# Kernel optimization log

Measured on AMD Instinct MI355X. Metric: run time of the kernel, lower is better.

Reference implementation:

```python
import jax, jax.numpy as jnp
import numpy as np


def setup_inputs() -> dict:
    key = jax.random.key(0)
    D, B, F_in, H = 8, 256, 64, 128  # depth, n_trees, n_node_features, n_hidden
    S = 2 ** D - 1                    # nodes per complete binary tree = 255
    N = B * S                         # 65280 total nodes
    # Tree structure (heap layout, root = local node 0; children of i are 2i+1, 2i+2)
    idx = np.arange(S)
    level = np.floor(np.log2(idx + 1)).astype(np.int64)      # 0 at root .. D-1 at leaves
    node_order_single = (D - 1) - level                       # leaves evaluated first (order 0)
    child_local = np.arange(1, S)
    parent_local = (child_local - 1) // 2
    offs = (np.arange(B) * S)[:, None]
    parent_g = (parent_local[None, :] + offs).reshape(-1)
    child_g = (child_local[None, :] + offs).reshape(-1)
    ks = jax.random.split(key, 8)

    def w(k, shp, fan_in):
        return (jax.random.normal(k, shp, jnp.float32) / np.sqrt(np.float32(fan_in)))

    return {
        "features": jax.random.normal(ks[0], (N, F_in), jnp.float32),
        "W_iou": w(ks[1], (F_in, 3 * H), F_in),
        "b_iou": jnp.zeros((3 * H,), jnp.float32),
        "U_iou": w(ks[2], (H, 3 * H), H),
        "W_f": w(ks[3], (F_in, H), F_in),
        "b_f": jnp.zeros((H,), jnp.float32),
        "U_f": w(ks[4], (H, H), H),
        "lin1_w": w(ks[5], (H, H), H),
        "lin1_b": jnp.zeros((H,), jnp.float32),
        "lin2_w": w(ks[6], (H, H), H),
        "lin2_b": jnp.zeros((H,), jnp.float32),
        "lin_w": w(ks[7], (H, 1), H),
        "lin_b": jnp.zeros((1,), jnp.float32),
        "node_order": jnp.asarray(np.tile(node_order_single, B), jnp.int32),
        "adjacency_list": jnp.asarray(np.stack([parent_g, child_g], axis=1), jnp.int32),
        "edge_order": jnp.asarray(np.tile(node_order_single[parent_local], B), jnp.int32),
        "n_levels": int(D),
        "n_trees": int(B),
    }


def reference(features, W_iou, b_iou, U_iou, W_f, b_f, U_f,
              lin1_w, lin1_b, lin2_w, lin2_b, lin_w, lin_b,
              node_order, adjacency_list, edge_order, n_levels, n_trees):
    N = features.shape[0]
    H = U_f.shape[0]
    parent = adjacency_list[:, 0]
    child = adjacency_list[:, 1]
    # input-to-gate projections are level-independent; compute once
    Wx_iou = features @ W_iou + b_iou   # [N, 3H]
    Wx_f = features @ W_f + b_f         # [N, H]
    h = jnp.zeros((N, H), features.dtype)
    c = jnp.zeros((N, H), features.dtype)
    for lvl in range(n_levels):  # n_levels is a static Python int
        nmask = (node_order == lvl)[:, None]
        if lvl == 0:
            iou = Wx_iou
            c_sum = jnp.zeros((N, H), features.dtype)
        else:
            emask = (edge_order == lvl)[:, None]
            child_h = jnp.where(emask, h[child], 0.0)
            h_sum = jax.ops.segment_sum(child_h, parent, num_segments=N)  # sum child h per parent
            iou = Wx_iou + h_sum @ U_iou
            f = jax.nn.sigmoid(Wx_f[parent] + h[child] @ U_f)             # per-edge forget gate
            fc = jnp.where(emask, f * c[child], 0.0)
            c_sum = jax.ops.segment_sum(fc, parent, num_segments=N)
        i, o, u = jnp.split(iou, 3, axis=1)
        c_new = jax.nn.sigmoid(i) * jnp.tanh(u) + c_sum
        h_new = jax.nn.sigmoid(o) * jnp.tanh(c_new)
        h = jnp.where(nmask, h_new, h)
        c = jnp.where(nmask, c_new, c)
    # unbatch by (equal) tree sizes and mean-pool per tree (use_root=False)
    S = N // n_trees
    x = h.reshape(n_trees, S, H).mean(axis=1)
    x = jax.nn.relu(x)                                   # dropout: identity in eval
    x = jax.nn.relu(x @ lin1_w + lin1_b)
    x = jax.nn.relu(x @ lin2_w + lin2_b)
    out = (x @ lin_w + lin_b).reshape(-1)                # torch.flatten(x)
    return out
```

## Files before the change

### kernel.cpp

```cpp
#include <hip/hip_runtime.h>
#include <hip/hip_bf16.h>
#include <math.h>

#define S_NODES 255
#define B_TREES 256
#define F_IN 64
#define H_DIM 128

typedef __attribute__((ext_vector_type(8))) short short8;
typedef __attribute__((ext_vector_type(4))) float f32x4;

__device__ __forceinline__ float fsig(float x) {
    float e = __expf(-x);
    return __builtin_amdgcn_rcpf(1.0f + e);
}
__device__ __forceinline__ float ftanh_(float x) {
    x = fminf(fmaxf(x, -15.0f), 15.0f);
    float e = __expf(2.0f * x);
    return (e - 1.0f) * __builtin_amdgcn_rcpf(e + 1.0f);
}
__device__ __forceinline__ unsigned short f2bf(float x) {
    union { __hip_bfloat16 b; unsigned short u; } v; v.b = __float2bfloat16(x); return v.u;
}
__device__ __forceinline__ float bf2f(unsigned short u) {
    union { unsigned int w; float f; } v; v.w = ((unsigned int)u) << 16; return v.f;
}
__device__ __forceinline__ unsigned int packsplit(float x) {
    unsigned short hi = f2bf(x);
    unsigned short lo = f2bf(x - bf2f(hi));
    return (unsigned)hi | ((unsigned)lo << 16);
}
__device__ __forceinline__ float unpacksplit(unsigned int u) {
    return bf2f((unsigned short)(u & 0xffffu)) + bf2f((unsigned short)(u >> 16));
}

__global__ __launch_bounds__(256) void prep_bt(
    const float* __restrict__ U_iou, const float* __restrict__ U_f,
    const float* __restrict__ W_iou, const float* __restrict__ W_f,
    unsigned short* __restrict__ Btu, unsigned short* __restrict__ Btl)
{
    int t = blockIdx.x * 256 + threadIdx.x;
    if (t < 512 * 192) {
        int k = t >> 9, n = t & 511;
        float v;
        if (k < 128) v = (n < 384) ? U_iou[k * 384 + n] : U_f[k * 128 + (n - 384)];
        else {
            int kf = k - 128;
            v = (n < 384) ? 0.5f * W_iou[kf * 384 + n] : W_f[kf * 128 + (n - 384)];
        }
        unsigned short hi = f2bf(v);
        Btu[n * 384 + k] = hi;
        Btu[n * 384 + 192 + k] = f2bf(v - bf2f(hi));
    } else {
        int t2 = t - 512 * 192;
        int k = t2 & 63, n = t2 >> 6;
        float v = W_iou[k * 384 + n];
        unsigned short hi = f2bf(v);
        Btl[n * 128 + k] = hi;
        Btl[n * 128 + 64 + k] = f2bf(v - bf2f(hi));
    }
}

__global__ __launch_bounds__(256) void pack_weights(
    const float* __restrict__ W_iou, const float* __restrict__ W_f,
    const float* __restrict__ U_iou, const float* __restrict__ U_f,
    float4* __restrict__ Wp, float4* __restrict__ Up)
{
    int t = blockIdx.x * 256 + threadIdx.x;
    if (t < F_IN * H_DIM) {
        int k = t >> 7, j = t & 127;
        Wp[t] = make_float4(W_iou[k * 384 + j], W_iou[k * 384 + 128 + j],
                            W_iou[k * 384 + 256 + j], W_f[k * H_DIM + j]);
    } else {
        int t2 = t - F_IN * H_DIM;
        int k = t2 >> 7, j = t2 & 127;
        Up[t2] = make_float4(U_iou[k * 384 + j], U_iou[k * 384 + 128 + j],
                             U_iou[k * 384 + 256 + j], U_f[k * H_DIM + j]);
    }
}

#define MFMA(a, b, c) __builtin_amdgcn_mfma_f32_16x16x32_bf16(a, b, c, 0, 0, 0)

__global__ __launch_bounds__(512, 2) void leafgemm(
    const float* __restrict__ feat, const unsigned short* __restrict__ Btl,
    const float* __restrict__ b_iou,
    float* __restrict__ c_out, unsigned int* __restrict__ h2out)
{
    __shared__ __align__(16) char Alb[64 * 272];
    const int tid = threadIdx.x;
    const int w = tid >> 6, l = tid & 63;
    const int l15 = l & 15, l4 = l >> 4;
    const int NB = blockIdx.x << 6;

    int nct[3];
    #pragma unroll
    for (int ct = 0; ct < 3; ++ct) nct[ct] = (ct << 7) + (w << 4) + l15;

    short8 Bh[2][3], Bl[2][3];
    #define LLOADB(buf, ss) { int chb = ((ss) << 2) + l4;                         \
        _Pragma("unroll") for (int ct = 0; ct < 3; ++ct) {                        \
            const char* bp = (const char*)Btl + (size_t)nct[ct] * 256 + (chb << 4); \
            Bh[buf][ct] = *(const short8*)(bp);                                   \
            Bl[buf][ct] = *(const short8*)(bp + 128); } }

    LLOADB(0, 0)

    {
        int row = tid >> 3, o = tid & 7;
        int leafidx = NB + row;
        int tree = leafidx >> 7;
        size_t grow = (size_t)(tree * S_NODES + 127 + (leafidx & 127));
        const float* fp = feat + grow * F_IN + (o << 3);
        float4 va = *(const float4*)(fp);
        float4 vb = *(const float4*)(fp + 4);
        float vv[8] = {va.x, va.y, va.z, va.w, vb.x, vb.y, vb.z, vb.w};
        unsigned int qh[4], ql[4];
        #pragma unroll
        for (int e = 0; e < 4; ++e) {
            unsigned short h0 = f2bf(vv[2*e]), h1 = f2bf(vv[2*e+1]);
            unsigned short s0 = f2bf(vv[2*e] - bf2f(h0));
            unsigned short s1 = f2bf(vv[2*e+1] - bf2f(h1));
            qh[e] = (unsigned)h0 | ((unsigned)h1 << 16);
            ql[e] = (unsigned)s0 | ((unsigned)s1 << 16);
        }
        char* arow = Alb + row * 272;
        *(uint4*)(arow + (o << 4)) = make_uint4(qh[0], qh[1], qh[2], qh[3]);
        *(uint4*)(arow + ((8 + o) << 4)) = make_uint4(ql[0], ql[1], ql[2], ql[3]);
    }
    __syncthreads();

    f32x4 acc[4][3];
    #pragma unroll
    for (int rt = 0; rt < 4; ++rt)
        #pragma unroll
        for (int ct = 0; ct < 3; ++ct) acc[rt][ct] = (f32x4){0,0,0,0};

    #pragma unroll
    for (int s = 0; s < 2; ++s) {
        const int cur = s & 1;
        if (s < 1) LLOADB(1, 1)
        int ch = (s << 2) + l4;
        short8 ah[4], al[4];
        #pragma unroll
        for (int rt = 0; rt < 4; ++rt) {
            const char* ap = Alb + (rt * 16 + l15) * 272;
            ah[rt] = *(const short8*)(ap + (ch << 4));
            al[rt] = *(const short8*)(ap + ((8 + ch) << 4));
        }
        #pragma unroll
        for (int ct = 0; ct < 3; ++ct)
            #pragma unroll
            for (int rt = 0; rt < 4; ++rt) {
                acc[rt][ct] = MFMA(ah[rt], Bh[cur][ct], acc[rt][ct]);
                acc[rt][ct] = MFMA(al[rt], Bh[cur][ct], acc[rt][ct]);
                acc[rt][ct] = MFMA(ah[rt], Bl[cur][ct], acc[rt][ct]);
            }
    }

    const int j = (w << 4) + l15;
    float bi = b_iou[j], bo = b_iou[128 + j], bu = b_iou[256 + j];
    #pragma unroll
    for (int rt = 0; rt < 4; ++rt)
        #pragma unroll
        for (int rr = 0; rr < 4; ++rr) {
            int leafrow = rt * 16 + (l4 << 2) + rr;
            int leafidx = NB + leafrow;
            int tree = leafidx >> 7;
            size_t grow = (size_t)(tree * S_NODES + 127 + (leafidx & 127));
            float iv = acc[rt][0][rr] + bi;
            float ov = acc[rt][1][rr] + bo;
            float uv = acc[rt][2][rr] + bu;
            float cn = fsig(iv) * ftanh_(uv);
            float hn = fsig(ov) * ftanh_(cn);
            c_out[grow * 128 + j] = cn;
            h2out[grow * 128 + j] = packsplit(hn);
        }
    #undef LLOADB
}

__global__ __launch_bounds__(512, 2) void ugemm(
    const float* __restrict__ feat, const unsigned int* __restrict__ h2,
    const unsigned short* __restrict__ Btu,
    const float* __restrict__ b_iou, const float* __restrict__ b_f,
    float* __restrict__ c_io, unsigned int* __restrict__ h2out,
    int Lstart, int Lbits)
{
    __shared__ __align__(16) char Alb[64 * 784];
    const int tid = threadIdx.x;
    const int w = tid >> 6, l = tid & 63;
    const int l15 = l & 15, l4 = l >> 4;
    const int NB = blockIdx.x << 5;
    const int mask = (1 << Lbits) - 1;

    int nct[4];
    #pragma unroll
    for (int ct = 0; ct < 4; ++ct)
        nct[ct] = ((ct < 3) ? (ct << 7) : 384) + (w << 4) + l15;

    short8 Bh[2][4], Bl[2][4];
    #define ULOADB(buf, ss) { int chb = ((ss) << 2) + l4;                         \
        _Pragma("unroll") for (int ct = 0; ct < 4; ++ct) {                        \
            const char* bp = (const char*)Btu + (size_t)nct[ct] * 768 + (chb << 4); \
            Bh[buf][ct] = *(const short8*)(bp);                                   \
            Bl[buf][ct] = *(const short8*)(bp + 384); } }

    ULOADB(0, 0)

    #pragma unroll
    for (int i = 0; i < 2; ++i) {
        int tsk = tid + (i << 9);
        int row = tsk >> 4, o = tsk & 15;
        int node = NB + (row >> 1);
        int tree = node >> Lbits;
        int local = Lstart + (node & mask);
        size_t growc = (size_t)(tree * S_NODES + 2 * local + 1 + (row & 1));
        const unsigned int* hp = h2 + growc * 128 + (o << 3);
        uint4 a = *(const uint4*)(hp);
        uint4 b = *(const uint4*)(hp + 4);
        uint4 vh, vl;
        vh.x = (a.x & 0xffffu) | (a.y << 16);
        vh.y = (a.z & 0xffffu) | (a.w << 16);
        vh.z = (b.x & 0xffffu) | (b.y << 16);
        vh.w = (b.z & 0xffffu) | (b.w << 16);
        vl.x = (a.x >> 16) | (a.y & 0xffff0000u);
        vl.y = (a.z >> 16) | (a.w & 0xffff0000u);
        vl.z = (b.x >> 16) | (b.y & 0xffff0000u);
        vl.w = (b.z >> 16) | (b.w & 0xffff0000u);
        char* arow = Alb + row * 784;
        *(uint4*)(arow + (o << 4)) = vh;
        *(uint4*)(arow + ((24 + o) << 4)) = vl;
    }
    {
        int t2 = tid;
        int row = t2 >> 3, o = t2 & 7;
        int node = NB + (row >> 1);
        int tree = node >> Lbits;
        int local = Lstart + (node & mask);
        size_t growp = (size_t)(tree * S_NODES + local);
        const float* fp = feat + growp * F_IN + (o << 3);
        float4 va = *(const float4*)(fp);
        float4 vb = *(const float4*)(fp + 4);
        float vv[8] = {va.x, va.y, va.z, va.w, vb.x, vb.y, vb.z, vb.w};
        unsigned int qh[4], ql[4];
        #pragma unroll
        for (int e = 0; e < 4; ++e) {
            unsigned short h0 = f2bf(vv[2*e]), h1 = f2bf(vv[2*e+1]);
            unsigned short s0 = f2bf(vv[2*e] - bf2f(h0));
            unsigned short s1 = f2bf(vv[2*e+1] - bf2f(h1));
            qh[e] = (unsigned)h0 | ((unsigned)h1 << 16);
            ql[e] = (unsigned)s0 | ((unsigned)s1 << 16);
        }
        char* arow = Alb + row * 784;
        *(uint4*)(arow + ((16 + o) << 4)) = make_uint4(qh[0], qh[1], qh[2], qh[3]);
        *(uint4*)(arow + ((40 + o) << 4)) = make_uint4(ql[0], ql[1], ql[2], ql[3]);
    }
    __syncthreads();

    f32x4 acc[4][4];
    #pragma unroll
    for (int rt = 0; rt < 4; ++rt)
        #pragma unroll
        for (int ct = 0; ct < 4; ++ct) acc[rt][ct] = (f32x4){0,0,0,0};

    #pragma unroll
    for (int s = 0; s < 6; ++s) {
        const int cur = s & 1;
        if (s < 5) ULOADB(cur ^ 1, s + 1)
        int ch = (s << 2) + l4;
        short8 ah[4], al[4];
        #pragma unroll
        for (int rt = 0; rt < 4; ++rt) {
            const char* ap = Alb + (rt * 16 + l15) * 784;
            ah[rt] = *(const short8*)(ap + (ch << 4));
            al[rt] = *(const short8*)(ap + ((24 + ch) << 4));
        }
        #pragma unroll
        for (int ct = 0; ct < 4; ++ct)
            #pragma unroll
            for (int rt = 0; rt < 4; ++rt) {
                acc[rt][ct] = MFMA(ah[rt], Bh[cur][ct], acc[rt][ct]);
                acc[rt][ct] = MFMA(al[rt], Bh[cur][ct], acc[rt][ct]);
                acc[rt][ct] = MFMA(ah[rt], Bl[cur][ct], acc[rt][ct]);
            }
    }

    const int j = (w << 4) + l15;
    float bi = b_iou[j], bo = b_iou[128 + j], bu = b_iou[256 + j], bfv = b_f[j];
    #pragma unroll
    for (int rt = 0; rt < 4; ++rt)
        #pragma unroll
        for (int p = 0; p < 2; ++p) {
            int m = rt * 8 + (l4 << 1) + p;
            int node = NB + m;
            int tree = node >> Lbits;
            int local = Lstart + (node & mask);
            size_t gp = (size_t)(tree * S_NODES + local);
            size_t gl = (size_t)(tree * S_NODES + 2 * local + 1);
            float iv = acc[rt][0][2*p] + acc[rt][0][2*p+1] + bi;
            float ov = acc[rt][1][2*p] + acc[rt][1][2*p+1] + bo;
            float uv = acc[rt][2][2*p] + acc[rt][2][2*p+1] + bu;
            float fl = fsig(acc[rt][3][2*p] + bfv);
            float fr = fsig(acc[rt][3][2*p+1] + bfv);
            float cl = c_io[gl * 128 + j];
            float cr = c_io[(gl + 1) * 128 + j];
            float cn = fsig(iv) * ftanh_(uv) + fl * cl + fr * cr;
            float hn = fsig(ov) * ftanh_(cn);
            c_io[gp * 128 + j] = cn;
            h2out[gp * 128 + j] = packsplit(hn);
        }
    #undef ULOADB
}

#define ULOOP(KB, KE, HLROW, HRROW)                                             \
    _Pragma("unroll 2")                                                         \
    for (int k4 = (KB); k4 < (KE); k4 += 4) {                                   \
        float4 u0 = Up[(k4 + 0) * H_DIM + j];                                   \
        float4 u1 = Up[(k4 + 1) * H_DIM + j];                                   \
        float4 u2 = Up[(k4 + 2) * H_DIM + j];                                   \
        float4 u3 = Up[(k4 + 3) * H_DIM + j];                                   \
        _Pragma("unroll")                                                       \
        for (int g = 0; g < G; ++g) {                                           \
            float4 hl4 = *reinterpret_cast<const float4*>((HLROW) + k4);        \
            float4 hr4 = *reinterpret_cast<const float4*>((HRROW) + k4);        \
            float hs_;                                                          \
            hs_ = hl4.x + hr4.x;                                                \
            acc_i[g] = fmaf(hs_, u0.x, acc_i[g]);                               \
            acc_o[g] = fmaf(hs_, u0.y, acc_o[g]);                               \
            acc_u[g] = fmaf(hs_, u0.z, acc_u[g]);                               \
            acc_fl[g] = fmaf(hl4.x, u0.w, acc_fl[g]);                           \
            acc_fr[g] = fmaf(hr4.x, u0.w, acc_fr[g]);                           \
            hs_ = hl4.y + hr4.y;                                                \
            acc_i[g] = fmaf(hs_, u1.x, acc_i[g]);                               \
            acc_o[g] = fmaf(hs_, u1.y, acc_o[g]);                               \
            acc_u[g] = fmaf(hs_, u1.z, acc_u[g]);                               \
            acc_fl[g] = fmaf(hl4.y, u1.w, acc_fl[g]);                           \
            acc_fr[g] = fmaf(hr4.y, u1.w, acc_fr[g]);                           \
            hs_ = hl4.z + hr4.z;                                                \
            acc_i[g] = fmaf(hs_, u2.x, acc_i[g]);                               \
            acc_o[g] = fmaf(hs_, u2.y, acc_o[g]);                               \
            acc_u[g] = fmaf(hs_, u2.z, acc_u[g]);                               \
            acc_fl[g] = fmaf(hl4.z, u2.w, acc_fl[g]);                           \
            acc_fr[g] = fmaf(hr4.z, u2.w, acc_fr[g]);                           \
            hs_ = hl4.w + hr4.w;                                                \
            acc_i[g] = fmaf(hs_, u3.x, acc_i[g]);                               \
            acc_o[g] = fmaf(hs_, u3.y, acc_o[g]);                               \
            acc_u[g] = fmaf(hs_, u3.z, acc_u[g]);                               \
            acc_fl[g] = fmaf(hl4.w, u3.w, acc_fl[g]);                           \
            acc_fr[g] = fmaf(hr4.w, u3.w, acc_fr[g]);                           \
        }                                                                       \
    }

#define WLOOP(FS, WITH_F)                                                       \
    _Pragma("unroll 2")                                                         \
    for (int k4 = 0; k4 < F_IN; k4 += 4) {                                      \
        float4 w0 = Wp[(k4 + 0) * H_DIM + j];                                   \
        float4 w1 = Wp[(k4 + 1) * H_DIM + j];                                   \
        float4 w2 = Wp[(k4 + 2) * H_DIM + j];                                   \
        float4 w3 = Wp[(k4 + 3) * H_DIM + j];                                   \
        _Pragma("unroll")                                                       \
        for (int g = 0; g < G; ++g) {                                           \
            float4 f4 = *reinterpret_cast<const float4*>((FS) + g * F_IN + k4); \
            acc_i[g] = fmaf(f4.x, w0.x, acc_i[g]);                              \
            acc_o[g] = fmaf(f4.x, w0.y, acc_o[g]);                              \
            acc_u[g] = fmaf(f4.x, w0.z, acc_u[g]);                              \
            if (WITH_F) acc_f[g] = fmaf(f4.x, w0.w, acc_f[g]);                  \
            acc_i[g] = fmaf(f4.y, w1.x, acc_i[g]);                              \
            acc_o[g] = fmaf(f4.y, w1.y, acc_o[g]);                              \
            acc_u[g] = fmaf(f4.y, w1.z, acc_u[g]);                              \
            if (WITH_F) acc_f[g] = fmaf(f4.y, w1.w, acc_f[g]);                  \
            acc_i[g] = fmaf(f4.z, w2.x, acc_i[g]);                              \
            acc_o[g] = fmaf(f4.z, w2.y, acc_o[g]);                              \
            acc_u[g] = fmaf(f4.z, w2.z, acc_u[g]);                              \
            if (WITH_F) acc_f[g] = fmaf(f4.z, w2.w, acc_f[g]);                  \
            acc_i[g] = fmaf(f4.w, w3.x, acc_i[g]);                              \
            acc_o[g] = fmaf(f4.w, w3.y, acc_o[g]);                              \
            acc_u[g] = fmaf(f4.w, w3.z, acc_u[g]);                              \
            if (WITH_F) acc_f[g] = fmaf(f4.w, w3.w, acc_f[g]);                  \
        }                                                                       \
    }

__global__ __launch_bounds__(256) void tree_top_kernel(
    const float* __restrict__ feat, const float4* __restrict__ Wp,
    const float* __restrict__ b_iou, const float4* __restrict__ Up,
    const float* __restrict__ b_f,
    unsigned int* __restrict__ h2g, float* __restrict__ c)
{
    const int tree = blockIdx.x;
    const int tid = threadIdx.x;
    const int j = tid & 127;
    const int grp = tid >> 7;

    __shared__ float h_s[31][H_DIM];
    __shared__ float c_s[31][H_DIM];
    __shared__ float feat_s[2 * 4 * F_IN];
    __shared__ float red5[5][H_DIM];

    for (int idx = tid; idx < 16 * H_DIM; idx += 256) {
        int loc = 15 + (idx >> 7);
        int col = idx & 127;
        size_t n = (size_t)(tree * S_NODES + loc);
        h_s[loc][col] = unpacksplit(h2g[n * H_DIM + col]);
        c_s[loc][col] = c[n * H_DIM + col];
    }
    __syncthreads();

    float bi = b_iou[j], bo = b_iou[128 + j], bu = b_iou[256 + j], bf = b_f[j];

    #define TOP_SLOT(G_, BASE_)                                                      \
    {                                                                                \
        constexpr int G = G_;                                                        \
        const int base = BASE_;                                                      \
        for (int idx = tid; idx < 2 * G * F_IN; idx += 256) {                        \
            int gg = idx >> 6, kk = idx & 63;                                        \
            int local = base + gg;                                                   \
            feat_s[idx] = feat[(size_t)(tree * S_NODES + local) * F_IN + kk];        \
        }                                                                            \
        __syncthreads();                                                             \
        float acc_i[G], acc_o[G], acc_u[G], acc_f[G], acc_fl[G], acc_fr[G];          \
        _Pragma("unroll")                                                            \
        for (int g = 0; g < G; ++g) {                                                \
            acc_i[g] = bi; acc_o[g] = bo; acc_u[g] = bu;                             \
            acc_f[g] = bf; acc_fl[g] = 0.f; acc_fr[g] = 0.f;                         \
        }                                                                            \
        const float* fs = feat_s + grp * G * F_IN;                                   \
        WLOOP(fs, true)                                                              \
        ULOOP(0, H_DIM, &h_s[2 * (base + grp * G + g) + 1][0],                       \
                         &h_s[2 * (base + grp * G + g) + 2][0])                      \
        _Pragma("unroll")                                                            \
        for (int g = 0; g < G; ++g) {                                                \
            int p = base + grp * G + g;                                              \
            float cl = c_s[2 * p + 1][j];                                            \
            float cr = c_s[2 * p + 2][j];                                            \
            float cn = fsig(acc_i[g]) * ftanh_(acc_u[g]);                            \
            float fl = fsig(acc_f[g] + acc_fl[g]);                                   \
            float fr = fsig(acc_f[g] + acc_fr[g]);                                   \
            cn = fmaf(fl, cl, fmaf(fr, cr, cn));                                     \
            float hn = fsig(acc_o[g]) * ftanh_(cn);                                  \
            h_s[p][j] = hn;                                                          \
            c_s[p][j] = cn;                                                          \
            h2g[(size_t)(tree * S_NODES + p) * H_DIM + j] = packsplit(hn);           \
        }                                                                            \
        __syncthreads();                                                             \
    }

    TOP_SLOT(4, 7)
    TOP_SLOT(2, 3)
    TOP_SLOT(1, 1)
    #undef TOP_SLOT

    {
        constexpr int G = 1;
        constexpr int KS = 44;
        if (tid < F_IN) feat_s[tid] = feat[(size_t)(tree * S_NODES) * F_IN + tid];
        __syncthreads();
        float acc_i[1], acc_o[1], acc_u[1], acc_f[1], acc_fl[1], acc_fr[1];
        if (grp == 0) {
            acc_i[0] = bi; acc_o[0] = bo; acc_u[0] = bu;
            acc_f[0] = bf; acc_fl[0] = 0.f; acc_fr[0] = 0.f;
            WLOOP(feat_s, true)
            ULOOP(0, KS, &h_s[1][0], &h_s[2][0])
        } else {
            acc_i[0] = 0.f; acc_o[0] = 0.f; acc_u[0] = 0.f;
            acc_f[0] = 0.f; acc_fl[0] = 0.f; acc_fr[0] = 0.f;
            ULOOP(KS, H_DIM, &h_s[1][0], &h_s[2][0])
        }
        __syncthreads();
        if (grp == 1) {
            red5[0][j] = acc_i[0];
            red5[1][j] = acc_o[0];
            red5[2][j] = acc_u[0];
            red5[3][j] = acc_fl[0];
            red5[4][j] = acc_fr[0];
        }
        __syncthreads();
        if (grp == 0) {
            acc_i[0] += red5[0][j];
            acc_o[0] += red5[1][j];
            acc_u[0] += red5[2][j];
            acc_fl[0] += red5[3][j];
            acc_fr[0] += red5[4][j];
            float cl = c_s[1][j], cr = c_s[2][j];
            float cn = fsig(acc_i[0]) * ftanh_(acc_u[0]);
            float fl = fsig(acc_f[0] + acc_fl[0]);
            float fr = fsig(acc_f[0] + acc_fr[0]);
            cn = fmaf(fl, cl, fmaf(fr, cr, cn));
            float hn = fsig(acc_o[0]) * ftanh_(cn);
            h2g[(size_t)(tree * S_NODES) * H_DIM + j] = packsplit(hn);
        }
    }
}

__global__ __launch_bounds__(512) void readout_kernel(
    const unsigned int* __restrict__ h2,
    const float* __restrict__ lin1_w, const float* __restrict__ lin1_b,
    const float* __restrict__ lin2_w, const float* __restrict__ lin2_b,
    const float* __restrict__ lin_w, const float* __restrict__ lin_b,
    float* __restrict__ out)
{
    const int b = blockIdx.x;
    const int tid = threadIdx.x;
    const int q = tid >> 7;
    const int j = tid & 127;
    const unsigned int* hb = h2 + (size_t)b * S_NODES * H_DIM;

    float s = 0.f;
    #pragma unroll 4
    for (int n = q; n < S_NODES; n += 4) s += unpacksplit(hb[n * H_DIM + j]);

    __shared__ float part[4][H_DIM];
    __shared__ float xs[H_DIM];
    __shared__ float ys[H_DIM];
    __shared__ float red[2];

    part[q][j] = s;
    __syncthreads();
    if (tid < 128) {
        float t = (part[0][j] + part[1][j] + part[2][j] + part[3][j]) * (1.0f / 255.0f);
        xs[j] = fmaxf(t, 0.f);
    }
    __syncthreads();
    if (tid < 128) {
        float a = lin1_b[j];
        #pragma unroll 4
        for (int k = 0; k < H_DIM; ++k) a = fmaf(xs[k], lin1_w[k * H_DIM + j], a);
        ys[j] = fmaxf(a, 0.f);
    }
    __syncthreads();
    if (tid < 128) {
        float z = lin2_b[j];
        #pragma unroll 4
        for (int k = 0; k < H_DIM; ++k) z = fmaf(ys[k], lin2_w[k * H_DIM + j], z);
        z = fmaxf(z, 0.f);
        float t = z * lin_w[j];
        #pragma unroll
        for (int off = 32; off > 0; off >>= 1) t += __shfl_down(t, off, 64);
        if ((j & 63) == 0) red[j >> 6] = t;
    }
    __syncthreads();
    if (tid == 0) out[b] = red[0] + red[1] + lin_b[0];
}

extern "C" void kernel_launch(void* const* d_in, const int* in_sizes, int n_in,
                              void* d_out, int out_size, void* d_ws, size_t ws_size,
                              hipStream_t stream)
{
    const float* feat   = (const float*)d_in[0];
    const float* W_iou  = (const float*)d_in[1];
    const float* b_iou  = (const float*)d_in[2];
    const float* U_iou  = (const float*)d_in[3];
    const float* W_f    = (const float*)d_in[4];
    const float* b_f    = (const float*)d_in[5];
    const float* U_f    = (const float*)d_in[6];
    const float* lin1_w = (const float*)d_in[7];
    const float* lin1_b = (const float*)d_in[8];
    const float* lin2_w = (const float*)d_in[9];
    const float* lin2_b = (const float*)d_in[10];
    const float* lin_w  = (const float*)d_in[11];
    const float* lin_b  = (const float*)d_in[12];
    float* out = (float*)d_out;

    char* wsb = (char*)d_ws;
    float4* Wp = (float4*)wsb;
    float4* Up = (float4*)(wsb + 131072);
    unsigned short* Btu = (unsigned short*)(wsb + 393216);
    unsigned short* Btl = (unsigned short*)(wsb + 786432);
    float* c  = (float*)(wsb + 884736);
    unsigned int* h2 = (unsigned int*)(wsb + 884736 + (size_t)33423360);

    prep_bt<<<480, 256, 0, stream>>>(U_iou, U_f, W_iou, W_f, Btu, Btl);
    pack_weights<<<96, 256, 0, stream>>>(W_iou, W_f, U_iou, U_f, Wp, Up);

    leafgemm<<<512, 512, 0, stream>>>(feat, Btl, b_iou, c, h2);

    ugemm<<<512, 512, 0, stream>>>(feat, h2, Btu, b_iou, b_f, c, h2, 63, 6);
    ugemm<<<256, 512, 0, stream>>>(feat, h2, Btu, b_iou, b_f, c, h2, 31, 5);
    ugemm<<<128, 512, 0, stream>>>(feat, h2, Btu, b_iou, b_f, c, h2, 15, 4);

    tree_top_kernel<<<B_TREES, 256, 0, stream>>>(feat, Wp, b_iou, Up, b_f, h2, c);

    readout_kernel<<<B_TREES, 512, 0, stream>>>(
        h2, lin1_w, lin1_b, lin2_w, lin2_b, lin_w, lin_b, out);
}
```

Measured before the change: 248.6 us.

## Replace scalar tree-top kernel with MFMA ugemm launches for upper levels

Removes the per-tree scalar FMA tree_top_kernel and the pack_weights kernel, and processes the top four levels with additional ugemm launches that use bf16 MFMA with hi/lo split precision. The B-matrix layout is changed to interleave hi and lo 16-byte chunks per k-chunk, and prep_bt now writes vectorized 32-byte chunks from fewer threads. The cost is four extra small launches with very few blocks (down to 8), which leaves most of the GPU idle during those levels, in exchange for faster matrix math and one fewer prep kernel.

```diff
diff --git a/kernel.cpp b/kernel.cpp
--- a/kernel.cpp
+++ b/kernel.cpp
@@ -40,43 +40,40 @@
     unsigned short* __restrict__ Btu, unsigned short* __restrict__ Btl)
 {
     int t = blockIdx.x * 256 + threadIdx.x;
-    if (t < 512 * 192) {
-        int k = t >> 9, n = t & 511;
-        float v;
-        if (k < 128) v = (n < 384) ? U_iou[k * 384 + n] : U_f[k * 128 + (n - 384)];
-        else {
-            int kf = k - 128;
-            v = (n < 384) ? 0.5f * W_iou[kf * 384 + n] : W_f[kf * 128 + (n - 384)];
-        }
-        unsigned short hi = f2bf(v);
-        Btu[n * 384 + k] = hi;
-        Btu[n * 384 + 192 + k] = f2bf(v - bf2f(hi));
+    float v[8];
+    char* dst;
+    if (t < 512 * 24) {
+        int n = t / 24, cidx = t - n * 24;
+        #pragma unroll
+        for (int e = 0; e < 8; ++e) {
+            int k = cidx * 8 + e;
+            float x;
+            if (k < 128) x = (n < 384) ? U_iou[k * 384 + n] : U_f[k * 128 + (n - 384)];
+            else {
+                int kf = k - 128;
+                x = (n < 384) ? 0.5f * W_iou[kf * 384 + n] : W_f[kf * 128 + (n - 384)];
+            }
+            v[e] = x;
+        }
+        dst = (char*)Btu + (size_t)n * 768 + cidx * 32;
     } else {
-        int t2 = t - 512 * 192;
-        int k = t2 & 63, n = t2 >> 6;
-        float v = W_iou[k * 384 + n];
-        unsigned short hi = f2bf(v);
-        Btl[n * 128 + k] = hi;
-        Btl[n * 128 + 64 + k] = f2bf(v - bf2f(hi));
-    }
-}
-
-__global__ __launch_bounds__(256) void pack_weights(
-    const float* __restrict__ W_iou, const float* __restrict__ W_f,
-    const float* __restrict__ U_iou, const float* __restrict__ U_f,
-    float4* __restrict__ Wp, float4* __restrict__ Up)
-{
-    int t = blockIdx.x * 256 + threadIdx.x;
-    if (t < F_IN * H_DIM) {
-        int k = t >> 7, j = t & 127;
-        Wp[t] = make_float4(W_iou[k * 384 + j], W_iou[k * 384 + 128 + j],
-                            W_iou[k * 384 + 256 + j], W_f[k * H_DIM + j]);
-    } else {
-        int t2 = t - F_IN * H_DIM;
-        int k = t2 >> 7, j = t2 & 127;
-        Up[t2] = make_float4(U_iou[k * 384 + j], U_iou[k * 384 + 128 + j],
-                             U_iou[k * 384 + 256 + j], U_f[k * H_DIM + j]);
-    }
+        int t2 = t - 512 * 24;
+        int n = t2 >> 3, cidx = t2 & 7;
+        #pragma unroll
+        for (int e = 0; e < 8; ++e) v[e] = W_iou[(cidx * 8 + e) * 384 + n];
+        dst = (char*)Btl + (size_t)n * 256 + cidx * 32;
+    }
+    unsigned int hi[4], lo[4];
+    #pragma unroll
+    for (int e = 0; e < 4; ++e) {
+        unsigned short h0 = f2bf(v[2*e]), h1 = f2bf(v[2*e+1]);
+        unsigned short s0 = f2bf(v[2*e] - bf2f(h0));
+        unsigned short s1 = f2bf(v[2*e+1] - bf2f(h1));
+        hi[e] = (unsigned)h0 | ((unsigned)h1 << 16);
+        lo[e] = (unsigned)s0 | ((unsigned)s1 << 16);
+    }
+    *(uint4*)dst = make_uint4(hi[0], hi[1], hi[2], hi[3]);
+    *(uint4*)(dst + 16) = make_uint4(lo[0], lo[1], lo[2], lo[3]);
 }
 
 #define MFMA(a, b, c) __builtin_amdgcn_mfma_f32_16x16x32_bf16(a, b, c, 0, 0, 0)
@@ -97,11 +94,11 @@
     for (int ct = 0; ct < 3; ++ct) nct[ct] = (ct << 7) + (w << 4) + l15;
 
     short8 Bh[2][3], Bl[2][3];
-    #define LLOADB(buf, ss) { int chb = ((ss) << 2) + l4;                         \
-        _Pragma("unroll") for (int ct = 0; ct < 3; ++ct) {                        \
-            const char* bp = (const char*)Btl + (size_t)nct[ct] * 256 + (chb << 4); \
-            Bh[buf][ct] = *(const short8*)(bp);                                   \
-            Bl[buf][ct] = *(const short8*)(bp + 128); } }
+    #define LLOADB(buf, ss) { int chb = ((ss) << 2) + l4;                           \
+        _Pragma("unroll") for (int ct = 0; ct < 3; ++ct) {                          \
+            const char* bp = (const char*)Btl + (size_t)nct[ct] * 256 + (chb << 5); \
+            Bh[buf][ct] = *(const short8*)(bp);                                     \
+            Bl[buf][ct] = *(const short8*)(bp + 16); } }
 
     LLOADB(0, 0)
 
@@ -198,11 +195,11 @@
         nct[ct] = ((ct < 3) ? (ct << 7) : 384) + (w << 4) + l15;
 
     short8 Bh[2][4], Bl[2][4];
-    #define ULOADB(buf, ss) { int chb = ((ss) << 2) + l4;                         \
-        _Pragma("unroll") for (int ct = 0; ct < 4; ++ct) {                        \
-            const char* bp = (const char*)Btu + (size_t)nct[ct] * 768 + (chb << 4); \
-            Bh[buf][ct] = *(const short8*)(bp);                                   \
-            Bl[buf][ct] = *(const short8*)(bp + 384); } }
+    #define ULOADB(buf, ss) { int chb = ((ss) << 2) + l4;                           \
+        _Pragma("unroll") for (int ct = 0; ct < 4; ++ct) {                          \
+            const char* bp = (const char*)Btu + (size_t)nct[ct] * 768 + (chb << 5); \
+            Bh[buf][ct] = *(const short8*)(bp);                                     \
+            Bl[buf][ct] = *(const short8*)(bp + 16); } }
 
     ULOADB(0, 0)
 
@@ -311,185 +308,6 @@
     #undef ULOADB
 }
 
-#define ULOOP(KB, KE, HLROW, HRROW)                                             \
-    _Pragma("unroll 2")                                                         \
-    for (int k4 = (KB); k4 < (KE); k4 += 4) {                                   \
-        float4 u0 = Up[(k4 + 0) * H_DIM + j];                                   \
-        float4 u1 = Up[(k4 + 1) * H_DIM + j];                                   \
-        float4 u2 = Up[(k4 + 2) * H_DIM + j];                                   \
-        float4 u3 = Up[(k4 + 3) * H_DIM + j];                                   \
-        _Pragma("unroll")                                                       \
-        for (int g = 0; g < G; ++g) {                                           \
-            float4 hl4 = *reinterpret_cast<const float4*>((HLROW) + k4);        \
-            float4 hr4 = *reinterpret_cast<const float4*>((HRROW) + k4);        \
-            float hs_;                                                          \
-            hs_ = hl4.x + hr4.x;                                                \
-            acc_i[g] = fmaf(hs_, u0.x, acc_i[g]);                               \
-            acc_o[g] = fmaf(hs_, u0.y, acc_o[g]);                               \
-            acc_u[g] = fmaf(hs_, u0.z, acc_u[g]);                               \
-            acc_fl[g] = fmaf(hl4.x, u0.w, acc_fl[g]);                           \
-            acc_fr[g] = fmaf(hr4.x, u0.w, acc_fr[g]);                           \
-            hs_ = hl4.y + hr4.y;                                                \
-            acc_i[g] = fmaf(hs_, u1.x, acc_i[g]);                               \
-            acc_o[g] = fmaf(hs_, u1.y, acc_o[g]);                               \
-            acc_u[g] = fmaf(hs_, u1.z, acc_u[g]);                               \
-            acc_fl[g] = fmaf(hl4.y, u1.w, acc_fl[g]);                           \
-            acc_fr[g] = fmaf(hr4.y, u1.w, acc_fr[g]);                           \
-            hs_ = hl4.z + hr4.z;                                                \
-            acc_i[g] = fmaf(hs_, u2.x, acc_i[g]);                               \
-            acc_o[g] = fmaf(hs_, u2.y, acc_o[g]);                               \
-            acc_u[g] = fmaf(hs_, u2.z, acc_u[g]);                               \
-            acc_fl[g] = fmaf(hl4.z, u2.w, acc_fl[g]);                           \
-            acc_fr[g] = fmaf(hr4.z, u2.w, acc_fr[g]);                           \
-            hs_ = hl4.w + hr4.w;                                                \
-            acc_i[g] = fmaf(hs_, u3.x, acc_i[g]);                               \
-            acc_o[g] = fmaf(hs_, u3.y, acc_o[g]);                               \
-            acc_u[g] = fmaf(hs_, u3.z, acc_u[g]);                               \
-            acc_fl[g] = fmaf(hl4.w, u3.w, acc_fl[g]);                           \
-            acc_fr[g] = fmaf(hr4.w, u3.w, acc_fr[g]);                           \
-        }                                                                       \
-    }
-
-#define WLOOP(FS, WITH_F)                                                       \
-    _Pragma("unroll 2")                                                         \
-    for (int k4 = 0; k4 < F_IN; k4 += 4) {                                      \
-        float4 w0 = Wp[(k4 + 0) * H_DIM + j];                                   \
-        float4 w1 = Wp[(k4 + 1) * H_DIM + j];                                   \
-        float4 w2 = Wp[(k4 + 2) * H_DIM + j];                                   \
-        float4 w3 = Wp[(k4 + 3) * H_DIM + j];                                   \
-        _Pragma("unroll")                                                       \
-        for (int g = 0; g < G; ++g) {                                           \
-            float4 f4 = *reinterpret_cast<const float4*>((FS) + g * F_IN + k4); \
-            acc_i[g] = fmaf(f4.x, w0.x, acc_i[g]);                              \
-            acc_o[g] = fmaf(f4.x, w0.y, acc_o[g]);                              \
-            acc_u[g] = fmaf(f4.x, w0.z, acc_u[g]);                              \
-            if (WITH_F) acc_f[g] = fmaf(f4.x, w0.w, acc_f[g]);                  \
-            acc_i[g] = fmaf(f4.y, w1.x, acc_i[g]);                              \
-            acc_o[g] = fmaf(f4.y, w1.y, acc_o[g]);                              \
-            acc_u[g] = fmaf(f4.y, w1.z, acc_u[g]);                              \
-            if (WITH_F) acc_f[g] = fmaf(f4.y, w1.w, acc_f[g]);                  \
-            acc_i[g] = fmaf(f4.z, w2.x, acc_i[g]);                              \
-            acc_o[g] = fmaf(f4.z, w2.y, acc_o[g]);                              \
-            acc_u[g] = fmaf(f4.z, w2.z, acc_u[g]);                              \
-            if (WITH_F) acc_f[g] = fmaf(f4.z, w2.w, acc_f[g]);                  \
-            acc_i[g] = fmaf(f4.w, w3.x, acc_i[g]);                              \
-            acc_o[g] = fmaf(f4.w, w3.y, acc_o[g]);                              \
-            acc_u[g] = fmaf(f4.w, w3.z, acc_u[g]);                              \
-            if (WITH_F) acc_f[g] = fmaf(f4.w, w3.w, acc_f[g]);                  \
-        }                                                                       \
-    }
-
-__global__ __launch_bounds__(256) void tree_top_kernel(
-    const float* __restrict__ feat, const float4* __restrict__ Wp,
-    const float* __restrict__ b_iou, const float4* __restrict__ Up,
-    const float* __restrict__ b_f,
-    unsigned int* __restrict__ h2g, float* __restrict__ c)
-{
-    const int tree = blockIdx.x;
-    const int tid = threadIdx.x;
-    const int j = tid & 127;
-    const int grp = tid >> 7;
-
-    __shared__ float h_s[31][H_DIM];
-    __shared__ float c_s[31][H_DIM];
-    __shared__ float feat_s[2 * 4 * F_IN];
-    __shared__ float red5[5][H_DIM];
-
-    for (int idx = tid; idx < 16 * H_DIM; idx += 256) {
-        int loc = 15 + (idx >> 7);
-        int col = idx & 127;
-        size_t n = (size_t)(tree * S_NODES + loc);
-        h_s[loc][col] = unpacksplit(h2g[n * H_DIM + col]);
-        c_s[loc][col] = c[n * H_DIM + col];
-    }
-    __syncthreads();
-
-    float bi = b_iou[j], bo = b_iou[128 + j], bu = b_iou[256 + j], bf = b_f[j];
-
-    #define TOP_SLOT(G_, BASE_)                                                      \
-    {                                                                                \
-        constexpr int G = G_;                                                        \
-        const int base = BASE_;                                                      \
-        for (int idx = tid; idx < 2 * G * F_IN; idx += 256) {                        \
-            int gg = idx >> 6, kk = idx & 63;                                        \
-            int local = base + gg;                                                   \
-            feat_s[idx] = feat[(size_t)(tree * S_NODES + local) * F_IN + kk];        \
-        }                                                                            \
-        __syncthreads();                                                             \
-        float acc_i[G], acc_o[G], acc_u[G], acc_f[G], acc_fl[G], acc_fr[G];          \
-        _Pragma("unroll")                                                            \
-        for (int g = 0; g < G; ++g) {                                                \
-            acc_i[g] = bi; acc_o[g] = bo; acc_u[g] = bu;                             \
-            acc_f[g] = bf; acc_fl[g] = 0.f; acc_fr[g] = 0.f;                         \
-        }                                                                            \
-        const float* fs = feat_s + grp * G * F_IN;                                   \
-        WLOOP(fs, true)                                                              \
-        ULOOP(0, H_DIM, &h_s[2 * (base + grp * G + g) + 1][0],                       \
-                         &h_s[2 * (base + grp * G + g) + 2][0])                      \
-        _Pragma("unroll")                                                            \
-        for (int g = 0; g < G; ++g) {                                                \
-            int p = base + grp * G + g;                                              \
-            float cl = c_s[2 * p + 1][j];                                            \
-            float cr = c_s[2 * p + 2][j];                                            \
-            float cn = fsig(acc_i[g]) * ftanh_(acc_u[g]);                            \
-            float fl = fsig(acc_f[g] + acc_fl[g]);                                   \
-            float fr = fsig(acc_f[g] + acc_fr[g]);                                   \
-            cn = fmaf(fl, cl, fmaf(fr, cr, cn));                                     \
-            float hn = fsig(acc_o[g]) * ftanh_(cn);                                  \
-            h_s[p][j] = hn;                                                          \
-            c_s[p][j] = cn;                                                          \
-            h2g[(size_t)(tree * S_NODES + p) * H_DIM + j] = packsplit(hn);           \
-        }                                                                            \
-        __syncthreads();                                                             \
-    }
-
-    TOP_SLOT(4, 7)
-    TOP_SLOT(2, 3)
-    TOP_SLOT(1, 1)
-    #undef TOP_SLOT
-
-    {
-        constexpr int G = 1;
-        constexpr int KS = 44;
-        if (tid < F_IN) feat_s[tid] = feat[(size_t)(tree * S_NODES) * F_IN + tid];
-        __syncthreads();
-        float acc_i[1], acc_o[1], acc_u[1], acc_f[1], acc_fl[1], acc_fr[1];
-        if (grp == 0) {
-            acc_i[0] = bi; acc_o[0] = bo; acc_u[0] = bu;
-            acc_f[0] = bf; acc_fl[0] = 0.f; acc_fr[0] = 0.f;
-            WLOOP(feat_s, true)
-            ULOOP(0, KS, &h_s[1][0], &h_s[2][0])
-        } else {
-            acc_i[0] = 0.f; acc_o[0] = 0.f; acc_u[0] = 0.f;
-            acc_f[0] = 0.f; acc_fl[0] = 0.f; acc_fr[0] = 0.f;
-            ULOOP(KS, H_DIM, &h_s[1][0], &h_s[2][0])
-        }
-        __syncthreads();
-        if (grp == 1) {
-            red5[0][j] = acc_i[0];
-            red5[1][j] = acc_o[0];
-            red5[2][j] = acc_u[0];
-            red5[3][j] = acc_fl[0];
-            red5[4][j] = acc_fr[0];
-        }
-        __syncthreads();
-        if (grp == 0) {
-            acc_i[0] += red5[0][j];
-            acc_o[0] += red5[1][j];
-            acc_u[0] += red5[2][j];
-            acc_fl[0] += red5[3][j];
-            acc_fr[0] += red5[4][j];
-            float cl = c_s[1][j], cr = c_s[2][j];
-            float cn = fsig(acc_i[0]) * ftanh_(acc_u[0]);
-            float fl = fsig(acc_f[0] + acc_fl[0]);
-            float fr = fsig(acc_f[0] + acc_fr[0]);
-            cn = fmaf(fl, cl, fmaf(fr, cr, cn));
-            float hn = fsig(acc_o[0]) * ftanh_(cn);
-            h2g[(size_t)(tree * S_NODES) * H_DIM + j] = packsplit(hn);
-        }
-    }
-}
-
 __global__ __launch_bounds__(512) void readout_kernel(
     const unsigned int* __restrict__ h2,
     const float* __restrict__ lin1_w, const float* __restrict__ lin1_b,
@@ -560,23 +378,22 @@
     float* out = (float*)d_out;
 
     char* wsb = (char*)d_ws;
-    float4* Wp = (float4*)wsb;
-    float4* Up = (float4*)(wsb + 131072);
-    unsigned short* Btu = (unsigned short*)(wsb + 393216);
-    unsigned short* Btl = (unsigned short*)(wsb + 786432);
-    float* c  = (float*)(wsb + 884736);
-    unsigned int* h2 = (unsigned int*)(wsb + 884736 + (size_t)33423360);
-
-    prep_bt<<<480, 256, 0, stream>>>(U_iou, U_f, W_iou, W_f, Btu, Btl);
-    pack_weights<<<96, 256, 0, stream>>>(W_iou, W_f, U_iou, U_f, Wp, Up);
+    unsigned short* Btu = (unsigned short*)wsb;
+    unsigned short* Btl = (unsigned short*)(wsb + 393216);
+    float* c  = (float*)(wsb + 524288);
+    unsigned int* h2 = (unsigned int*)(wsb + 524288 + (size_t)33423360);
+
+    prep_bt<<<60, 256, 0, stream>>>(U_iou, U_f, W_iou, W_f, Btu, Btl);
 
     leafgemm<<<512, 512, 0, stream>>>(feat, Btl, b_iou, c, h2);
 
     ugemm<<<512, 512, 0, stream>>>(feat, h2, Btu, b_iou, b_f, c, h2, 63, 6);
     ugemm<<<256, 512, 0, stream>>>(feat, h2, Btu, b_iou, b_f, c, h2, 31, 5);
     ugemm<<<128, 512, 0, stream>>>(feat, h2, Btu, b_iou, b_f, c, h2, 15, 4);
-
-    tree_top_kernel<<<B_TREES, 256, 0, stream>>>(feat, Wp, b_iou, Up, b_f, h2, c);
+    ugemm<<<64,  512, 0, stream>>>(feat, h2, Btu, b_iou, b_f, c, h2,  7, 3);
+    ugemm<<<32,  512, 0, stream>>>(feat, h2, Btu, b_iou, b_f, c, h2,  3, 2);
+    ugemm<<<16,  512, 0, stream>>>(feat, h2, Btu, b_iou, b_f, c, h2,  1, 1);
+    ugemm<<<8,   512, 0, stream>>>(feat, h2, Btu, b_iou, b_f, c, h2,  0, 0);
 
     readout_kernel<<<B_TREES, 512, 0, stream>>>(
         h2, lin1_w, lin1_b, lin2_w, lin2_b, lin_w, lin_b, out);
```

Measured after the change: 271.7 us. 9.3% more time.
